# Kernel optimization log

Hardware: AMD Instinct MI355X
Metric: run time of the kernel (lower is better)

## Reference

```python
import jax, jax.numpy as jnp
import numpy as np

B, N, S, E = 64, 200_000, 6, 1_000_000   # batch, nodes, steps, edges-per-step
N_IN, N_OUT = 4096, 1024                 # input node ids = [0, N_IN), output ids = [N-N_OUT, N)


def setup_inputs() -> dict:
    key = jax.random.key(0)
    k0, k1, k2, k3, k4 = jax.random.split(key, 5)
    x = jax.random.normal(k0, (B, N_IN), dtype=jnp.float32)
    w_in = jnp.ones((N_IN,), dtype=jnp.float32)            # Linear(1,1) on inputs, init to 1.0
    bias = jax.random.normal(k1, (N,), dtype=jnp.float32)  # per-node bias
    w_edge = jax.random.normal(k2, (S, E), dtype=jnp.float32)  # per-edge Linear(1,1) weight
    src = jax.random.randint(k3, (S, E), 0, N)             # edge sources, per step
    dst = jax.random.randint(k4, (S, E), 0, N)             # edge destinations, per step
    return {"x": x, "w_in": w_in, "bias": bias, "w_edge": w_edge, "src": src, "dst": dst}


def reference(x, w_in, bias, w_edge, src, dst):
    n_nodes = bias.shape[0]
    n_in = x.shape[1]
    n_steps = w_edge.shape[0]
    act = jnp.tanh

    # node-major state [N, B] so segment ops run over the leading axis
    state = jnp.zeros((n_nodes, x.shape[0]), dtype=x.dtype)

    # input phase: state[i] = act(w_in[i]*x[:,i] + bias[i] + state[i]); state starts at 0
    s_in = act(x * w_in[None, :] + bias[None, :n_in])       # [B, N_IN]
    state = state.at[:n_in, :].set(s_in.T)

    ones_e = jnp.ones((src.shape[1],), dtype=x.dtype)
    for step in range(n_steps):  # fixed, small step count (max_steps)
        # per-edge scalar message: w * state[src]  -> [E, B]
        contrib = w_edge[step][:, None] * state[src[step]]
        msg = jax.ops.segment_sum(contrib, dst[step], num_segments=n_nodes)      # [N, B]
        fan_in = jax.ops.segment_sum(ones_e, dst[step], num_segments=n_nodes)    # [N]
        # only nodes with incoming edges this step are updated (temp_states semantics)
        new_state = act(msg + bias[:, None] + state)
        state = jnp.where((fan_in > 0)[:, None], new_state, state)

    # return output-node states, batch-major: [B, N_OUT]
    return state[n_nodes - N_OUT:, :].T
```

## Files before the change

kernel.cpp:

```cpp
#include <hip/hip_runtime.h>
#include <hip/hip_fp16.h>

#define NB      64
#define NNODES  200000
#define NSTEPS  6
#define NEDGES  1000000
#define NIN     4096
#define NOUT    1024
#define NC      391
#define NCP     512
#define CWID    512
#define CAPC    3072
#define CHUNK   8000
#define CPS     125
#define NODESP  (NC * CWID)

__global__ void input_kernel(const float* __restrict__ x,
                             const float* __restrict__ w_in,
                             const float* __restrict__ bias,
                             __half* __restrict__ A0) {
    int tid = blockIdx.x * blockDim.x + threadIdx.x;
    int i = tid >> 6;
    int b = tid & 63;
    if (i >= NIN) return;
    float v = tanhf(x[(size_t)b * NIN + i] * w_in[i] + bias[i]);
    A0[(size_t)i * NB + b] = __float2half(v);
}

__global__ __launch_bounds__(256) void pass1_kernel(
        const int* __restrict__ dst,
        int* __restrict__ gcnt,
        unsigned* __restrict__ stage1) {
    __shared__ unsigned staged[CHUNK];
    __shared__ int hist[NCP], excl[NCP], cur[NCP], gbase[NC];
    __shared__ int wsum[4];
    int t = threadIdx.x, lane = t & 63, wid = t >> 6;
    int s = blockIdx.x / CPS;
    int chunk = blockIdx.x - s * CPS;
    int e0 = chunk * CHUNK;
    const int* dstS = dst + (size_t)s * NEDGES;

    hist[t] = 0; hist[t + 256] = 0;
    __syncthreads();
    for (int i = t; i < CHUNK; i += 256)
        atomicAdd(&hist[dstS[e0 + i] >> 9], 1);
    __syncthreads();

    int a = hist[2 * t], b = hist[2 * t + 1];
    int pair = a + b, v = pair;
    for (int off = 1; off < 64; off <<= 1) {
        int u = __shfl_up(v, off);
        if (lane >= off) v += u;
    }
    if (lane == 63) wsum[wid] = v;
    __syncthreads();
    int woff = 0;
    for (int w2 = 0; w2 < wid; w2++) woff += wsum[w2];
    int epair = v - pair + woff;
    excl[2 * t] = epair;         cur[2 * t] = epair;
    excl[2 * t + 1] = epair + a; cur[2 * t + 1] = epair + a;
    __syncthreads();

    for (int i = t; i < CHUNK; i += 256) {
        int d = dstS[e0 + i];
        int pos = atomicAdd(&cur[d >> 9], 1);
        staged[pos] = ((unsigned)(d & 511) << 20) | (unsigned)(e0 + i);
    }
    __syncthreads();

    for (int c = t; c < NC; c += 256) {
        int len = hist[c];
        gbase[c] = len ? atomicAdd(&gcnt[s * NCP + c], len) : 0;
    }
    __syncthreads();
    for (int c = wid; c < NC; c += 4) {
        int len = hist[c];
        if (!len) continue;
        int st = excl[c], gb = gbase[c];
        int room = CAPC - gb; if (room < 0) room = 0;
        if (len > room) len = room;
        unsigned* g = stage1 + ((size_t)(s * NC + c)) * CAPC + gb;
        for (int j = lane; j < len; j += 64) g[j] = staged[st + j];
    }
}

__global__ __launch_bounds__(256) void pass2_kernel(
        const unsigned* __restrict__ stage1S,
        const int* __restrict__ gcntS,
        const int* __restrict__ srcS,
        const float* __restrict__ wS,
        uint2* __restrict__ finalR,
        uint2* __restrict__ off2S) {
    __shared__ unsigned staged[CAPC];
    __shared__ int hist[CWID], excl[CWID], cur[CWID];
    __shared__ int wsum[4];
    int t = threadIdx.x, lane = t & 63, wid = t >> 6;
    int c = blockIdx.x;
    int m = gcntS[c]; if (m > CAPC) m = CAPC;
    const unsigned* g = stage1S + (size_t)c * CAPC;

    hist[t] = 0; hist[t + 256] = 0;
    __syncthreads();
    for (int i = t; i < m; i += 256) {
        unsigned r = g[i];
        staged[i] = r;
        atomicAdd(&hist[r >> 20], 1);
    }
    __syncthreads();

    int a = hist[2 * t], b = hist[2 * t + 1];
    int pair = a + b, v = pair;
    for (int off = 1; off < 64; off <<= 1) {
        int u = __shfl_up(v, off);
        if (lane >= off) v += u;
    }
    if (lane == 63) wsum[wid] = v;
    __syncthreads();
    int woff = 0;
    for (int w2 = 0; w2 < wid; w2++) woff += wsum[w2];
    int epair = v - pair + woff;
    excl[2 * t] = epair;         cur[2 * t] = epair;
    excl[2 * t + 1] = epair + a; cur[2 * t + 1] = epair + a;
    __syncthreads();

    int base = c * CAPC;
    for (int dl = t; dl < CWID; dl += 256) {
        int s1 = base + excl[dl];
        off2S[c * CWID + dl] = make_uint2((unsigned)s1, (unsigned)(s1 + hist[dl]));
    }

    for (int i = t; i < m; i += 256) {
        unsigned r = staged[i];
        int dl = (int)(r >> 20);
        int el = (int)(r & 0xFFFFFu);
        int pos = base + atomicAdd(&cur[dl], 1);
        finalR[pos] = make_uint2((unsigned)srcS[el], __float_as_uint(wS[el]));
    }
}

__global__ __launch_bounds__(256) void pull_kernel(
        const float* __restrict__ bias,
        const uint2* __restrict__ rec,
        const uint2* __restrict__ off2S,
        const __half* __restrict__ Aold,
        __half* __restrict__ Anew) {
    int gw = (int)((blockIdx.x * 256 + threadIdx.x) >> 6);
    int lane = threadIdx.x & 63;
    int n = __builtin_amdgcn_readfirstlane(gw);
    if (n >= NNODES) return;
    size_t row = ((size_t)n << 6) | lane;
    __half aold = Aold[row];
    uint2 o = off2S[n];
    if (o.x == o.y) { Anew[row] = aold; return; }
    float acc = __half2float(aold) + bias[n];
    for (unsigned k = o.x; k < o.y; ++k) {
        uint2 q = rec[k];
        acc += __uint_as_float(q.y) *
               __half2float(Aold[((size_t)q.x << 6) | lane]);
    }
    Anew[row] = __float2half(tanhf(acc));
}

__global__ void output_kernel(const __half* __restrict__ A,
                              float* __restrict__ out) {
    int tid = blockIdx.x * blockDim.x + threadIdx.x;
    if (tid >= NB * NOUT) return;
    int b = tid / NOUT;
    int j = tid % NOUT;
    out[tid] = __half2float(A[(size_t)(NNODES - NOUT + j) * NB + b]);
}

extern "C" void kernel_launch(void* const* d_in, const int* in_sizes, int n_in,
                              void* d_out, int out_size, void* d_ws, size_t ws_size,
                              hipStream_t stream) {
    const float* x      = (const float*)d_in[0];
    const float* w_in   = (const float*)d_in[1];
    const float* bias   = (const float*)d_in[2];
    const float* w_edge = (const float*)d_in[3];
    const int*   src    = (const int*)d_in[4];
    const int*   dst    = (const int*)d_in[5];
    float* out = (float*)d_out;

    char* p = (char*)d_ws;
    __half*   A0     = (__half*)p;   p += (size_t)NNODES * NB * 2;
    __half*   A1     = (__half*)p;   p += (size_t)NNODES * NB * 2;
    int*      gcnt   = (int*)p;      p += (size_t)NSTEPS * NCP * 4;
    unsigned* stage1 = (unsigned*)p; p += (size_t)NSTEPS * NC * CAPC * 4;
    uint2*    finalR = (uint2*)p;    p += (size_t)NC * CAPC * 8;
    uint2*    off2   = (uint2*)p;

    hipMemsetAsync(A0, 0, (size_t)NNODES * NB * 2, stream);
    hipMemsetAsync(gcnt, 0, (size_t)NSTEPS * NCP * 4, stream);

    input_kernel<<<(NIN * NB + 255) / 256, 256, 0, stream>>>(x, w_in, bias, A0);

    pass1_kernel<<<NSTEPS * CPS, 256, 0, stream>>>(dst, gcnt, stage1);

    const int pblocks = (NNODES * NB) / 256;
    __half* curA = A0; __half* nxtA = A1;
    for (int s = 0; s < NSTEPS; ++s) {
        pass2_kernel<<<NC, 256, 0, stream>>>(
            stage1 + (size_t)s * NC * CAPC,
            gcnt + (size_t)s * NCP,
            src + (size_t)s * NEDGES,
            w_edge + (size_t)s * NEDGES,
            finalR,
            off2 + (size_t)s * NODESP);
        pull_kernel<<<pblocks, 256, 0, stream>>>(
            bias, finalR, off2 + (size_t)s * NODESP, curA, nxtA);
        __half* tmp = curA; curA = nxtA; nxtA = tmp;
    }

    output_kernel<<<(NB * NOUT + 255) / 256, 256, 0, stream>>>(curA, out);
}
```

Before: 809.9 us.

## Process two nodes per wavefront, restrict last step to output nodes, skip zero sources

The pull kernel now handles two nodes per wavefront and interleaves their edge loops, giving more independent gathers in flight. On the last step only the output nodes (and their pass2 chunks) are computed, since other node states are never read. On step 0 gathers from sources outside the input range are skipped because those states are known to be zero. The loss is extra branching and imbalance when the two nodes have very different fan-in.

```diff
diff --git a/kernel.cpp b/kernel.cpp
--- a/kernel.cpp
+++ b/kernel.cpp
@@ -90,12 +90,13 @@
         const int* __restrict__ srcS,
         const float* __restrict__ wS,
         uint2* __restrict__ finalR,
-        uint2* __restrict__ off2S) {
+        uint2* __restrict__ off2S,
+        int cBase) {
     __shared__ unsigned staged[CAPC];
     __shared__ int hist[CWID], excl[CWID], cur[CWID];
     __shared__ int wsum[4];
     int t = threadIdx.x, lane = t & 63, wid = t >> 6;
-    int c = blockIdx.x;
+    int c = blockIdx.x + cBase;
     int m = gcntS[c]; if (m > CAPC) m = CAPC;
     const unsigned* g = stage1S + (size_t)c * CAPC;
 
@@ -143,22 +144,35 @@
         const uint2* __restrict__ rec,
         const uint2* __restrict__ off2S,
         const __half* __restrict__ Aold,
-        __half* __restrict__ Anew) {
+        __half* __restrict__ Anew,
+        int nodeBase, int nodeEnd, int srcLimit) {
     int gw = (int)((blockIdx.x * 256 + threadIdx.x) >> 6);
     int lane = threadIdx.x & 63;
-    int n = __builtin_amdgcn_readfirstlane(gw);
-    if (n >= NNODES) return;
-    size_t row = ((size_t)n << 6) | lane;
-    __half aold = Aold[row];
-    uint2 o = off2S[n];
-    if (o.x == o.y) { Anew[row] = aold; return; }
-    float acc = __half2float(aold) + bias[n];
-    for (unsigned k = o.x; k < o.y; ++k) {
-        uint2 q = rec[k];
-        acc += __uint_as_float(q.y) *
-               __half2float(Aold[((size_t)q.x << 6) | lane]);
-    }
-    Anew[row] = __float2half(tanhf(acc));
+    int n0 = nodeBase + 2 * __builtin_amdgcn_readfirstlane(gw);
+    if (n0 >= nodeEnd) return;
+    int n1 = n0 + 1;
+    size_t row0 = ((size_t)n0 << 6) | lane;
+    size_t row1 = row0 + NB;
+    __half a0 = Aold[row0], a1 = Aold[row1];
+    uint2 o0 = off2S[n0], o1 = off2S[n1];
+    bool upd0 = (o0.x != o0.y), upd1 = (o1.x != o1.y);
+    float acc0 = __half2float(a0) + bias[n0];
+    float acc1 = __half2float(a1) + bias[n1];
+    unsigned k0 = o0.x, k1 = o1.x;
+    while (k0 < o0.y || k1 < o1.y) {
+        bool h0 = k0 < o0.y, h1 = k1 < o1.y;
+        uint2 q0, q1;
+        float g0 = 0.f, g1 = 0.f;
+        if (h0) q0 = rec[k0++];
+        if (h1) q1 = rec[k1++];
+        if (h0 && (int)q0.x < srcLimit)
+            g0 = __uint_as_float(q0.y) * __half2float(Aold[((size_t)q0.x << 6) | lane]);
+        if (h1 && (int)q1.x < srcLimit)
+            g1 = __uint_as_float(q1.y) * __half2float(Aold[((size_t)q1.x << 6) | lane]);
+        acc0 += g0; acc1 += g1;
+    }
+    Anew[row0] = upd0 ? __float2half(tanhf(acc0)) : a0;
+    Anew[row1] = upd1 ? __float2half(tanhf(acc1)) : a1;
 }
 
 __global__ void output_kernel(const __half* __restrict__ A,
@@ -196,18 +210,25 @@
 
     pass1_kernel<<<NSTEPS * CPS, 256, 0, stream>>>(dst, gcnt, stage1);
 
-    const int pblocks = (NNODES * NB) / 256;
     __half* curA = A0; __half* nxtA = A1;
     for (int s = 0; s < NSTEPS; ++s) {
-        pass2_kernel<<<NC, 256, 0, stream>>>(
+        bool last = (s == NSTEPS - 1);
+        int cBase   = last ? (NNODES - NOUT) >> 9 : 0;
+        int cBlocks = last ? NC - cBase : NC;
+        pass2_kernel<<<cBlocks, 256, 0, stream>>>(
             stage1 + (size_t)s * NC * CAPC,
             gcnt + (size_t)s * NCP,
             src + (size_t)s * NEDGES,
             w_edge + (size_t)s * NEDGES,
             finalR,
-            off2 + (size_t)s * NODESP);
-        pull_kernel<<<pblocks, 256, 0, stream>>>(
-            bias, finalR, off2 + (size_t)s * NODESP, curA, nxtA);
+            off2 + (size_t)s * NODESP,
+            cBase);
+        int nodeBase = last ? NNODES - NOUT : 0;
+        int nodeCnt  = last ? NOUT : NNODES;
+        int srcLimit = (s == 0) ? NIN : NNODES;
+        pull_kernel<<<nodeCnt / 8, 256, 0, stream>>>(
+            bias, finalR, off2 + (size_t)s * NODESP, curA, nxtA,
+            nodeBase, nodeBase + nodeCnt, srcLimit);
         __half* tmp = curA; curA = nxtA; nxtA = tmp;
     }
 
```

Result: faster. 671.7 us (-17.1%).
